# Kernel tuning notes

Hardware: AMD Instinct MI355X
Metric: run time of the kernel (lower is better)

## Reference

```python
import jax, jax.numpy as jnp
import numpy as np

# ---- constant lookup tables (mirror SoftALU registered buffers) ----
def _build_tables():
    n = np.arange(16)
    A, Bq, C = np.meshgrid(n, n, np.arange(2), indexing='ij')
    total = A + Bq + C
    eye16 = np.eye(16, dtype=np.float32)
    eye2 = np.eye(2, dtype=np.float32)
    add_t = eye16[total % 16]        # (16,16,2,16)
    carry_t = eye2[total // 16]      # (16,16,2,2)
    and_t = eye16[n[:, None] & n[None, :]]
    or_t = eye16[n[:, None] | n[None, :]]
    xor_t = eye16[n[:, None] ^ n[None, :]]
    bb = np.arange(256)
    b2n = np.zeros((256, 32), np.float32)
    b2n[bb, bb >> 4] = 1.0
    b2n[bb, 16 + (bb & 15)] = 1.0
    return tuple(jnp.asarray(t) for t in (add_t, carry_t, and_t, or_t, xor_t, b2n, b2n.T))

ADD_T, CARRY_T, AND_T, OR_T, XOR_T, B2N, N2B = _build_tables()
_SHIFTS = jnp.arange(4, dtype=jnp.uint32) * jnp.uint32(8)
SHARP = 100.0  # softmax sharpening temperature from the original module


def _sharp(x):
    return jax.nn.softmax(SHARP * x, axis=-1)


def _to_nibbles(x):  # x: (B,4,256) -> (high, low) each (B,4,16)
    comb = jnp.einsum('bnc,cm->bnm', x, B2N)
    return _sharp(comb[..., :16]), _sharp(comb[..., 16:])


def _from_nibbles(high, low):  # (...,16),(...,16) -> (...,256)
    return _sharp(jnp.einsum('...m,mc->...c', jnp.concatenate([high, low], axis=-1), N2B))


def _nibble_add(a, b, cin):  # (B,16),(B,16),(B,2) -> sum (B,16), carry (B,2)
    w = jnp.einsum('bi,bj,bk->bijk', a, b, cin)
    s = jnp.einsum('bijk,ijkl->bl', w, ADD_T)
    c = jnp.einsum('bijk,ijkl->bl', w, CARRY_T)
    return _sharp(s), _sharp(c)


def soft_add(a, b):  # (B,4,256) x2 -> (B,4,256), little-endian ripple-carry over 8 nibbles
    ah, al = _to_nibbles(a)
    bh, bl = _to_nibbles(b)
    carry = jnp.broadcast_to(jnp.array([1.0, 0.0], dtype=a.dtype), (a.shape[0], 2))
    out = []
    for i in range(4):  # fixed 4-byte carry recurrence (structural, not data dim)
        s_lo, carry = _nibble_add(al[:, i], bl[:, i], carry)
        s_hi, carry = _nibble_add(ah[:, i], bh[:, i], carry)
        out.append(_from_nibbles(s_hi, s_lo))
    return jnp.stack(out, axis=1)


def soft_bitwise(a, b, table):
    ah, al = _to_nibbles(a)
    bh, bl = _to_nibbles(b)
    r_hi = _sharp(jnp.einsum('bni,bnj,ijk->bnk', ah, bh, table))
    r_lo = _sharp(jnp.einsum('bni,bnj,ijk->bnk', al, bl, table))
    return _from_nibbles(r_hi, r_lo)


def _encode_u32(v):  # (B,) uint32 -> (B,4,256) one-hot bytes (little-endian)
    bytes_ = (v[:, None] >> _SHIFTS) & jnp.uint32(255)
    return jax.nn.one_hot(bytes_, 256, dtype=jnp.float32)


def _decode_u32(x):  # (B,4,256) -> (B,) uint32 (argmax decode, as in module.decode)
    bytes_ = jnp.argmax(x, axis=-1).astype(jnp.uint32)
    return (bytes_ << _SHIFTS).sum(axis=-1).astype(jnp.uint32)


def soft_negate(x):  # two's complement: xor with 0xFF per byte, then +1
    xh, xl = _to_nibbles(x)
    xf = XOR_T[:, 15, :]  # xor-with-0xF map (0xF is an exact one-hot in the original)
    f_hi = _sharp(jnp.einsum('bni,ik->bnk', xh, xf))
    f_lo = _sharp(jnp.einsum('bni,ik->bnk', xl, xf))
    flipped = _from_nibbles(f_hi, f_lo)
    one = _encode_u32(jnp.ones((x.shape[0],), dtype=jnp.uint32))
    return soft_add(flipped, one)


def soft_mul(a, b):
    # Original: decode -> silu(a)*b + silu(-a)*(-b) == exact a*b -> round -> encode.
    # Exact integer product mod 2^32 (encode masks to 32 bits).
    return _encode_u32(_decode_u32(a) * _decode_u32(b))


def soft_div(a, b):
    # decode() yields unsigned 0..2^32-1, so the original's repeated-subtraction
    # loop computes unsigned integer division, with b==0 -> 0.
    av, bv = _decode_u32(a), _decode_u32(b)
    q = jnp.where(bv == jnp.uint32(0), jnp.uint32(0), av // jnp.maximum(bv, jnp.uint32(1)))
    return _encode_u32(q)


def setup_inputs() -> dict:
    key = jax.random.key(0)
    k1, k2 = jax.random.split(key)
    Bsz = 8192
    a = jax.nn.one_hot(jax.random.randint(k1, (Bsz, 4), 0, 256), 256, dtype=jnp.float32)
    b = jax.nn.one_hot(jax.random.randint(k2, (Bsz, 4), 0, 256), 256, dtype=jnp.float32)
    return {"a": a, "b": b}


def reference(a, b):
    # all_ops(): (add, sub, mul, div, and, or, xor) each (B,4,256) -> (7,B,4,256)
    return jnp.stack([
        soft_add(a, b),
        soft_add(a, soft_negate(b)),  # subtract = a + (~b + 1)
        soft_mul(a, b),
        soft_div(a, b),
        soft_bitwise(a, b, AND_T),
        soft_bitwise(a, b, OR_T),
        soft_bitwise(a, b, XOR_T),
    ], axis=0)
```

## Files before the change

### kernel.cpp

```cpp
#include <hip/hip_runtime.h>
#include <stdint.h>


typedef float vfloat4 __attribute__((ext_vector_type(4)));

__global__ __launch_bounds__(256) void decode_kernel(const float* __restrict__ a,
                                                     const float* __restrict__ b,
                                                     uint32_t* __restrict__ res,
                                                     int B) {
    const int batch = blockIdx.x;
    const int t = threadIdx.x;

    __shared__ uint32_t sh_bytes[8];

    const float* pa = a + (size_t)batch * 1024;
    const float* pb = b + (size_t)batch * 1024;
#pragma unroll
    for (int n = 0; n < 4; ++n) {
        if (pa[n * 256 + t] > 0.5f) sh_bytes[n] = (uint32_t)t;
        if (pb[n * 256 + t] > 0.5f) sh_bytes[4 + n] = (uint32_t)t;
    }
    __syncthreads();

    if (t == 0) {
        const uint32_t av = sh_bytes[0] | (sh_bytes[1] << 8) | (sh_bytes[2] << 16) | (sh_bytes[3] << 24);
        const uint32_t bv = sh_bytes[4] | (sh_bytes[5] << 8) | (sh_bytes[6] << 16) | (sh_bytes[7] << 24);
        res[0 * B + batch] = av + bv;
        res[1 * B + batch] = av - bv;
        res[2 * B + batch] = av * bv;
        res[3 * B + batch] = bv ? (av / bv) : 0u;
        res[4 * B + batch] = av & bv;
        res[5 * B + batch] = av | bv;
        res[6 * B + batch] = av ^ bv;
    }
}

__global__ __launch_bounds__(256) void writer_kernel(const uint32_t* __restrict__ res,
                                                     vfloat4* __restrict__ out,
                                                     int B) {
    const size_t total = (size_t)7 * B * 4 * 64;
    const size_t stride = (size_t)gridDim.x * blockDim.x;
    for (size_t g = (size_t)blockIdx.x * blockDim.x + threadIdx.x; g < total; g += stride) {
        const int lane4 = (int)(g & 63);
        const size_t row = g >> 6;
        const int n = (int)(row & 3);
        const int ob = __builtin_amdgcn_readfirstlane((int)(row >> 2));
        const uint32_t r = res[ob];
        const int rb = (int)((r >> (8 * n)) & 255u);
        const int c0 = lane4 * 4;
        vfloat4 v;
        v.x = (c0 + 0 == rb) ? 1.0f : 0.0f;
        v.y = (c0 + 1 == rb) ? 1.0f : 0.0f;
        v.z = (c0 + 2 == rb) ? 1.0f : 0.0f;
        v.w = (c0 + 3 == rb) ? 1.0f : 0.0f;
        __builtin_nontemporal_store(v, &out[g]);
    }
}

extern "C" void kernel_launch(void* const* d_in, const int* in_sizes, int n_in,
                              void* d_out, int out_size, void* d_ws, size_t ws_size,
                              hipStream_t stream) {
    const float* a = (const float*)d_in[0];
    const float* b = (const float*)d_in[1];
    float* out = (float*)d_out;
    const int B = in_sizes[0] / (4 * 256);
    uint32_t* res = (uint32_t*)d_ws;

    decode_kernel<<<B, 256, 0, stream>>>(a, b, res, B);
    writer_kernel<<<4096, 256, 0, stream>>>(res, (vfloat4*)out, B);
}
```

Before: 289.8 us.

## Fuse decode and one-hot writer into a single per-batch kernel

Merges the decode kernel and the grid-stride writer kernel into one launch. Each block loads its batch rows as float4 vectors, decodes the bytes, computes the seven results into shared memory, and writes the seven one-hot outputs directly. This removes the second launch and the workspace round-trip, and halves the load instructions in decode. The cost is a second barrier per block and 8192 small blocks doing the writes instead of a persistent grid.

```diff
diff --git a/kernel.cpp b/kernel.cpp
--- a/kernel.cpp
+++ b/kernel.cpp
@@ -4,56 +4,57 @@
 
 typedef float vfloat4 __attribute__((ext_vector_type(4)));
 
-__global__ __launch_bounds__(256) void decode_kernel(const float* __restrict__ a,
+__global__ __launch_bounds__(256) void softalu_fused(const float* __restrict__ a,
                                                      const float* __restrict__ b,
-                                                     uint32_t* __restrict__ res,
+                                                     vfloat4* __restrict__ out,
                                                      int B) {
     const int batch = blockIdx.x;
     const int t = threadIdx.x;
 
     __shared__ uint32_t sh_bytes[8];
+    __shared__ uint32_t res7[7];
 
-    const float* pa = a + (size_t)batch * 1024;
-    const float* pb = b + (size_t)batch * 1024;
-#pragma unroll
-    for (int n = 0; n < 4; ++n) {
-        if (pa[n * 256 + t] > 0.5f) sh_bytes[n] = (uint32_t)t;
-        if (pb[n * 256 + t] > 0.5f) sh_bytes[4 + n] = (uint32_t)t;
-    }
+    const vfloat4* a4 = (const vfloat4*)a + (size_t)batch * 256;
+    const vfloat4* b4 = (const vfloat4*)b + (size_t)batch * 256;
+    const vfloat4 va = a4[t];
+    const vfloat4 vb = b4[t];
+
+    const int n = t >> 6;
+    const int c0 = (t & 63) * 4;
+
+    if (va.x > 0.5f) sh_bytes[n] = (uint32_t)(c0 + 0);
+    if (va.y > 0.5f) sh_bytes[n] = (uint32_t)(c0 + 1);
+    if (va.z > 0.5f) sh_bytes[n] = (uint32_t)(c0 + 2);
+    if (va.w > 0.5f) sh_bytes[n] = (uint32_t)(c0 + 3);
+    if (vb.x > 0.5f) sh_bytes[4 + n] = (uint32_t)(c0 + 0);
+    if (vb.y > 0.5f) sh_bytes[4 + n] = (uint32_t)(c0 + 1);
+    if (vb.z > 0.5f) sh_bytes[4 + n] = (uint32_t)(c0 + 2);
+    if (vb.w > 0.5f) sh_bytes[4 + n] = (uint32_t)(c0 + 3);
     __syncthreads();
 
     if (t == 0) {
         const uint32_t av = sh_bytes[0] | (sh_bytes[1] << 8) | (sh_bytes[2] << 16) | (sh_bytes[3] << 24);
         const uint32_t bv = sh_bytes[4] | (sh_bytes[5] << 8) | (sh_bytes[6] << 16) | (sh_bytes[7] << 24);
-        res[0 * B + batch] = av + bv;
-        res[1 * B + batch] = av - bv;
-        res[2 * B + batch] = av * bv;
-        res[3 * B + batch] = bv ? (av / bv) : 0u;
-        res[4 * B + batch] = av & bv;
-        res[5 * B + batch] = av | bv;
-        res[6 * B + batch] = av ^ bv;
+        res7[0] = av + bv;
+        res7[1] = av - bv;
+        res7[2] = av * bv;
+        res7[3] = bv ? (av / bv) : 0u;
+        res7[4] = av & bv;
+        res7[5] = av | bv;
+        res7[6] = av ^ bv;
     }
-}
+    __syncthreads();
 
-__global__ __launch_bounds__(256) void writer_kernel(const uint32_t* __restrict__ res,
-                                                     vfloat4* __restrict__ out,
-                                                     int B) {
-    const size_t total = (size_t)7 * B * 4 * 64;
-    const size_t stride = (size_t)gridDim.x * blockDim.x;
-    for (size_t g = (size_t)blockIdx.x * blockDim.x + threadIdx.x; g < total; g += stride) {
-        const int lane4 = (int)(g & 63);
-        const size_t row = g >> 6;
-        const int n = (int)(row & 3);
-        const int ob = __builtin_amdgcn_readfirstlane((int)(row >> 2));
-        const uint32_t r = res[ob];
+#pragma unroll
+    for (int op = 0; op < 7; ++op) {
+        const uint32_t r = res7[op];
         const int rb = (int)((r >> (8 * n)) & 255u);
-        const int c0 = lane4 * 4;
         vfloat4 v;
         v.x = (c0 + 0 == rb) ? 1.0f : 0.0f;
         v.y = (c0 + 1 == rb) ? 1.0f : 0.0f;
         v.z = (c0 + 2 == rb) ? 1.0f : 0.0f;
         v.w = (c0 + 3 == rb) ? 1.0f : 0.0f;
-        __builtin_nontemporal_store(v, &out[g]);
+        __builtin_nontemporal_store(v, &out[((size_t)op * B + batch) * 256 + t]);
     }
 }
 
@@ -62,10 +63,7 @@
                               hipStream_t stream) {
     const float* a = (const float*)d_in[0];
     const float* b = (const float*)d_in[1];
-    float* out = (float*)d_out;
     const int B = in_sizes[0] / (4 * 256);
-    uint32_t* res = (uint32_t*)d_ws;
-
-    decode_kernel<<<B, 256, 0, stream>>>(a, b, res, B);
-    writer_kernel<<<4096, 256, 0, stream>>>(res, (vfloat4*)out, B);
+    (void)d_ws; (void)ws_size;
+    softalu_fused<<<B, 256, 0, stream>>>(a, b, (vfloat4*)d_out, B);
 }
```

New measurement: 287.5 us. About the same (-0.8%).
